# Performance work log

Hardware: AMD Instinct MI355X
Metric: run time of the kernel (lower is better)

## Reference

```python
import jax, jax.numpy as jnp
import numpy as np

D_MODEL = 1024
N_HEADS = 16
D_HEAD = D_MODEL // N_HEADS


def setup_inputs() -> dict:
    key = jax.random.key(0)
    ks = jax.random.split(key, 9)
    B, S = 2, 2048
    s = 0.02
    return {
        "x": jax.random.normal(ks[0], (B, S, D_MODEL), dtype=jnp.float32),
        "Wq": jax.random.normal(ks[1], (D_MODEL, D_MODEL), dtype=jnp.float32) * s,
        "bq": jnp.zeros((D_MODEL,), dtype=jnp.float32),
        "Wk": jax.random.normal(ks[2], (D_MODEL, D_MODEL), dtype=jnp.float32) * s,
        "bk": jnp.zeros((D_MODEL,), dtype=jnp.float32),
        "Wv": jax.random.normal(ks[3], (D_MODEL, D_MODEL), dtype=jnp.float32) * s,
        "bv": jnp.zeros((D_MODEL,), dtype=jnp.float32),
        "Wo": jax.random.normal(ks[4], (D_MODEL, D_MODEL), dtype=jnp.float32) * s,
        "bo": jnp.zeros((D_MODEL,), dtype=jnp.float32),
    }


def reference(x, Wq, bq, Wk, bk, Wv, bv, Wo, bo):
    B, S, _ = x.shape
    # projections -> [B, H, S, Dh]
    def split_heads(t):
        return t.reshape(B, S, N_HEADS, D_HEAD).transpose(0, 2, 1, 3)
    Q = split_heads(x @ Wq + bq)
    K = split_heads(x @ Wk + bk)
    V = split_heads(x @ Wv + bv)
    scores = jnp.einsum('bhqd,bhkd->bhqk', Q, K)  # [B,H,S,S]
    mask = jnp.tril(jnp.ones((S, S), dtype=bool))
    # NB: original masks BEFORE scaling (mask fill -1e9 then /sqrt(d_head))
    scores = jnp.where(mask[None, None], scores, jnp.float32(-1e9))
    scores = scores / jnp.sqrt(jnp.float32(D_HEAD))
    attn = jax.nn.softmax(scores, axis=-1)
    ctx = jnp.einsum('bhqk,bhkd->bhqd', attn, V)
    ctx = ctx.transpose(0, 2, 1, 3).reshape(B, S, D_MODEL)
    return ctx @ Wo + bo
```

## Files before the change

kernel.cpp:

```cpp
#include <hip/hip_runtime.h>

typedef __bf16 bf16;
typedef __bf16 bf16x8 __attribute__((ext_vector_type(8)));
typedef __bf16 bf16x4 __attribute__((ext_vector_type(4)));
typedef float  f32x4  __attribute__((ext_vector_type(4)));

#define D_MODEL 1024
#define S_LEN   2048
#define NHEAD   16
#define DHEAD   64
#define BATCH   2
#define MROWS   (BATCH * S_LEN)

#define QSCALE 0.18033688011112042f

__device__ __forceinline__ void gld_lds16(const void* g, void* lds_base) {
    __builtin_amdgcn_global_load_lds(
        (const __attribute__((address_space(1))) void*)g,
        (__attribute__((address_space(3))) void*)lds_base, 16, 0, 0);
}

__global__ void prep_kernel(const float* __restrict__ x,
                            const float* __restrict__ W0, const float* __restrict__ W1,
                            const float* __restrict__ W2, const float* __restrict__ W3,
                            bf16* __restrict__ xb, bf16* __restrict__ Wt) {
    int tx = threadIdx.x, ty = threadIdx.y;
    if (blockIdx.z == 4) {
        int tid = ty * 32 + tx;
        size_t base = ((size_t)blockIdx.y * 32 + blockIdx.x) * 4096;
#pragma unroll
        for (int j = 0; j < 4; j++) {
            size_t i = base + (size_t)(j * 256 + tid) * 4;
            f32x4 v = *(const f32x4*)(x + i);
            bf16x4 o;
            o[0] = (bf16)v[0]; o[1] = (bf16)v[1]; o[2] = (bf16)v[2]; o[3] = (bf16)v[3];
            *(bf16x4*)(xb + i) = o;
        }
        return;
    }
    __shared__ float tile[32][33];
    const float* W = (blockIdx.z == 0) ? W0 : (blockIdx.z == 1) ? W1
                   : (blockIdx.z == 2) ? W2 : W3;
    int n0 = blockIdx.x * 32, k0 = blockIdx.y * 32;
#pragma unroll
    for (int j = 0; j < 4; j++)
        tile[ty + 8 * j][tx] = W[(size_t)(k0 + ty + 8 * j) * D_MODEL + n0 + tx];
    __syncthreads();
    bf16* out = Wt + (size_t)blockIdx.z * D_MODEL * D_MODEL;
#pragma unroll
    for (int j = 0; j < 4; j++)
        out[(size_t)(n0 + ty + 8 * j) * D_MODEL + k0 + tx] = (bf16)tile[tx][ty + 8 * j];
}

template <int MODE>
__global__ __launch_bounds__(256, 3) void gemm_kernel(
    const bf16* __restrict__ A, const bf16* __restrict__ Bt,
    const float* __restrict__ b0, const float* __restrict__ b1, const float* __restrict__ b2,
    bf16* __restrict__ Qo, bf16* __restrict__ Ko, bf16* __restrict__ Vto,
    float* __restrict__ Co) {
    constexpr int BN = (MODE == 0) ? 128 : 64;
    constexpr int MI = (MODE == 0) ? 4 : 2;
    __shared__ bf16 sA[3][128 * 32];
    __shared__ bf16 sB[3][BN * 32];
    const int t = threadIdx.x;
    const int wave = t >> 6, lane = t & 63;
    const int quad = lane >> 4, m16 = lane & 15;
    const int wrow = (MODE == 0) ? (wave >> 1) * 64 : wave * 32;
    const int wcol = (MODE == 0) ? (wave & 1) * 64 : 0;
    const int row0 = blockIdx.y * 128, col0 = blockIdx.x * BN;
    const int K = D_MODEL;
    constexpr int NK = D_MODEL / 32;

    f32x4 acc[MI][4];
#pragma unroll
    for (int i = 0; i < MI; i++)
#pragma unroll
        for (int j = 0; j < 4; j++) acc[i][j] = (f32x4){0.f, 0.f, 0.f, 0.f};

    auto stage = [&](int kk, int buf) {
#pragma unroll
        for (int i = 0; i < 2; i++) {
            int cb = i * 256 + wave * 64;
            int c  = cb + lane;
            int r  = c >> 2, kg = c & 3;
            int gk = kg ^ ((r >> 1) & 3);
            gld_lds16(A + (size_t)(row0 + r) * K + kk * 32 + gk * 8,
                      (char*)&sA[buf][0] + cb * 16);
        }
#pragma unroll
        for (int i = 0; i < BN / 64; i++) {
            int cb = i * 256 + wave * 64;
            int c  = cb + lane;
            int r  = c >> 2, kg = c & 3;
            int gk = kg ^ ((r >> 1) & 3);
            gld_lds16(Bt + (size_t)(col0 + r) * K + kk * 32 + gk * 8,
                      (char*)&sB[buf][0] + cb * 16);
        }
    };

    stage(0, 0);
    stage(1, 1);

    const int sx = (m16 >> 1) & 3;
    for (int ks = 0; ks < NK; ++ks) {
        if (ks + 1 < NK) {
            if constexpr (MODE == 0)
                asm volatile("s_waitcnt vmcnt(4)\n\ts_barrier" ::: "memory");
            else
                asm volatile("s_waitcnt vmcnt(3)\n\ts_barrier" ::: "memory");
        } else {
            asm volatile("s_waitcnt vmcnt(0)\n\ts_barrier" ::: "memory");
        }
        if (ks + 2 < NK) stage(ks + 2, (ks + 2) % 3);

        const int cur = ks % 3;
        const int gg = (quad ^ sx) * 8;
        bf16x8 af[MI], bfr[4];
#pragma unroll
        for (int mi = 0; mi < MI; mi++)
            af[mi] = *(const bf16x8*)&sA[cur][(wrow + mi * 16 + m16) * 32 + gg];
#pragma unroll
        for (int ni = 0; ni < 4; ni++)
            bfr[ni] = *(const bf16x8*)&sB[cur][(wcol + ni * 16 + m16) * 32 + gg];
#pragma unroll
        for (int mi = 0; mi < MI; mi++)
#pragma unroll
            for (int ni = 0; ni < 4; ni++)
                acc[mi][ni] = __builtin_amdgcn_mfma_f32_16x16x32_bf16(
                    af[mi], bfr[ni], acc[mi][ni], 0, 0, 0);
    }

    if (MODE == 1) {
#pragma unroll
        for (int mi = 0; mi < MI; mi++) {
            int r0 = row0 + wrow + mi * 16 + quad * 4;
#pragma unroll
            for (int ni = 0; ni < 4; ni++) {
                int col = col0 + wcol + ni * 16 + m16;
                float bias = b0[col];
#pragma unroll
                for (int r = 0; r < 4; r++)
                    Co[(size_t)(r0 + r) * D_MODEL + col] = acc[mi][ni][r] + bias;
            }
        }
    } else {
        int sel = col0 >> 10;
        const float* bias_arr = (sel == 0) ? b0 : (sel == 1) ? b1 : b2;
#pragma unroll
        for (int mi = 0; mi < MI; mi++) {
            int s0g = row0 + wrow + mi * 16 + quad * 4;
            int b = s0g >> 11, ss0 = s0g & 2047;
#pragma unroll
            for (int ni = 0; ni < 4; ni++) {
                int col = col0 + wcol + ni * 16 + m16;
                int cn = col & 1023;
                int h = cn >> 6, d = cn & 63;
                float bias = bias_arr[cn];
                if (sel < 2) {
                    bf16* dst = (sel == 0) ? Qo : Ko;
                    float scl = (sel == 0) ? QSCALE : 1.0f;
                    size_t base = (((size_t)b * NHEAD + h) * S_LEN);
#pragma unroll
                    for (int r = 0; r < 4; r++)
                        dst[(base + ss0 + r) * DHEAD + d] = (bf16)((acc[mi][ni][r] + bias) * scl);
                } else {
                    bf16x4 pk;
#pragma unroll
                    for (int r = 0; r < 4; r++) pk[r] = (bf16)(acc[mi][ni][r] + bias);
                    *(bf16x4*)(Vto + (((size_t)b * NHEAD + h) * DHEAD + d) * S_LEN + ss0) = pk;
                }
            }
        }
    }
}

__global__ __launch_bounds__(256, 4) void attn_kernel(
    const bf16* __restrict__ Q, const bf16* __restrict__ K,
    const bf16* __restrict__ Vt, bf16* __restrict__ ctx) {
    __shared__ bf16 Kt_s[2][64 * 64];
    __shared__ bf16 Vt_s[2][64 * 64];

    const int t = threadIdx.x, wave = t >> 6, lane = t & 63;
    const int quad = lane >> 4, m16 = lane & 15;
    const int bh = blockIdx.x;
    const int qt = 31 - blockIdx.y;
    const int nt = qt + 1;
    const size_t base = (size_t)bh * S_LEN * DHEAD;

    bf16x8 aq[2];
#pragma unroll
    for (int kst = 0; kst < 2; kst++)
        aq[kst] = *(const bf16x8*)(Q + base
            + (size_t)(qt * 64 + wave * 16 + m16) * DHEAD + kst * 32 + quad * 8);

    f32x4 o[4];
#pragma unroll
    for (int di = 0; di < 4; di++) o[di] = (f32x4){0.f, 0.f, 0.f, 0.f};
    float l_acc = 0.f;

    auto stage = [&](int j, int buf) {
#pragma unroll
        for (int i = 0; i < 2; i++) {
            int cb = i * 256 + wave * 64;
            int c  = cb + lane;
            int pos = c >> 3, g = c & 7;
            int gk = g ^ (pos & 7);
            gld_lds16(K  + base + (size_t)(j * 64 + pos) * DHEAD + gk * 8,
                      (char*)&Kt_s[buf][0] + cb * 16);
            gld_lds16(Vt + base + (size_t)pos * S_LEN + j * 64 + gk * 8,
                      (char*)&Vt_s[buf][0] + cb * 16);
        }
    };

    stage(0, 0);

    for (int j = 0; j < nt; ++j) {
        asm volatile("s_waitcnt vmcnt(0)\n\ts_barrier" ::: "memory");
        if (j + 1 < nt) stage(j + 1, (j + 1) & 1);

        const int cur = j & 1;
        const int kt0 = j * 64;

        f32x4 sc[4];
#pragma unroll
        for (int ni = 0; ni < 4; ni++) sc[ni] = (f32x4){0.f, 0.f, 0.f, 0.f};
        __builtin_amdgcn_s_setprio(1);
#pragma unroll
        for (int ni = 0; ni < 4; ni++) {
            int pos = ni * 16 + m16;
#pragma unroll
            for (int kst = 0; kst < 2; kst++) {
                int gg = (kst * 4 + quad) ^ (pos & 7);
                bf16x8 kf = *(const bf16x8*)&Kt_s[cur][pos * 64 + gg * 8];
                sc[ni] = __builtin_amdgcn_mfma_f32_16x16x32_bf16(
                    kf, aq[kst], sc[ni], 0, 0, 0);
            }
        }
        __builtin_amdgcn_s_setprio(0);

        if (j == qt) {
            int qg = qt * 64 + wave * 16 + m16;
#pragma unroll
            for (int ni = 0; ni < 4; ni++)
#pragma unroll
                for (int r = 0; r < 4; r++) {
                    int kp = kt0 + ni * 16 + quad * 4 + r;
                    if (kp > qg) sc[ni][r] = -1e9f;
                }
        }

        unsigned int pd[4][2];
        {
            float ls0 = 0.f, ls1 = 0.f;
#pragma unroll
            for (int ni = 0; ni < 4; ni++) {
                float p0 = __builtin_amdgcn_exp2f(sc[ni][0]);
                float p1 = __builtin_amdgcn_exp2f(sc[ni][1]);
                float p2 = __builtin_amdgcn_exp2f(sc[ni][2]);
                float p3 = __builtin_amdgcn_exp2f(sc[ni][3]);
                union { bf16x4 h; unsigned int u[2]; } cv;
                cv.h[0] = (bf16)p0; cv.h[1] = (bf16)p1;
                cv.h[2] = (bf16)p2; cv.h[3] = (bf16)p3;
                pd[ni][0] = cv.u[0];
                pd[ni][1] = cv.u[1];
                ls0 += p0 + p1;
                ls1 += p2 + p3;
            }
            l_acc += ls0 + ls1;
        }

#pragma unroll
        for (int kst = 0; kst < 2; kst++) {
            unsigned int x0 = pd[2 * kst][0],     y0 = pd[2 * kst][1];
            unsigned int x1 = pd[2 * kst + 1][0], y1 = pd[2 * kst + 1][1];
            asm("v_permlane32_swap_b32 %0, %1" : "+v"(x0), "+v"(x1));
            asm("v_permlane32_swap_b32 %0, %1" : "+v"(y0), "+v"(y1));
            asm("v_permlane16_swap_b32 %0, %1" : "+v"(x0), "+v"(x1));
            asm("v_permlane16_swap_b32 %0, %1" : "+v"(y0), "+v"(y1));
            union { unsigned int u[4]; bf16x8 v; } pk;
            pk.u[0] = x0; pk.u[1] = y0; pk.u[2] = x1; pk.u[3] = y1;
            bf16x8 ap = pk.v;
            __builtin_amdgcn_s_setprio(1);
#pragma unroll
            for (int di = 0; di < 4; di++) {
                int d = di * 16 + m16;
                int gg = (kst * 4 + quad) ^ (d & 7);
                bf16x8 vf = *(const bf16x8*)&Vt_s[cur][d * 64 + gg * 8];
                o[di] = __builtin_amdgcn_mfma_f32_16x16x32_bf16(
                    vf, ap, o[di], 0, 0, 0);
            }
            __builtin_amdgcn_s_setprio(0);
        }
    }

    int b = bh >> 4, h = bh & 15;
    float l = l_acc;
    l += __shfl_xor(l, 16);
    l += __shfl_xor(l, 32);
    float rl = 1.0f / l;
    int s = qt * 64 + wave * 16 + m16;
#pragma unroll
    for (int di = 0; di < 4; di++) {
        bf16x4 pk;
#pragma unroll
        for (int r = 0; r < 4; r++) pk[r] = (bf16)(o[di][r] * rl);
        *(bf16x4*)(ctx + ((size_t)b * S_LEN + s) * D_MODEL
                   + h * DHEAD + di * 16 + quad * 4) = pk;
    }
}

extern "C" void kernel_launch(void* const* d_in, const int* in_sizes, int n_in,
                              void* d_out, int out_size, void* d_ws, size_t ws_size,
                              hipStream_t stream) {
    const float* x  = (const float*)d_in[0];
    const float* Wq = (const float*)d_in[1];
    const float* bq = (const float*)d_in[2];
    const float* Wk = (const float*)d_in[3];
    const float* bk = (const float*)d_in[4];
    const float* Wv = (const float*)d_in[5];
    const float* bv = (const float*)d_in[6];
    const float* Wo = (const float*)d_in[7];
    const float* bo = (const float*)d_in[8];
    float* out = (float*)d_out;

    char* ws = (char*)d_ws;
    const size_t MB = 1u << 20;
    bf16* xb  = (bf16*)(ws + 0);
    bf16* Wt  = (bf16*)(ws + 8  * MB);
    bf16* Qb  = (bf16*)(ws + 16 * MB);
    bf16* Kb  = (bf16*)(ws + 24 * MB);
    bf16* Vtb = (bf16*)(ws + 32 * MB);
    bf16* ctx = (bf16*)(ws + 0);

    prep_kernel<<<dim3(32, 32, 5), dim3(32, 8), 0, stream>>>(x, Wq, Wk, Wv, Wo, xb, Wt);
    gemm_kernel<0><<<dim3(24, 32), 256, 0, stream>>>(xb, Wt, bq, bk, bv,
                                                     Qb, Kb, Vtb, nullptr);
    attn_kernel<<<dim3(32, 32), 256, 0, stream>>>(Qb, Kb, Vtb, ctx);
    gemm_kernel<1><<<dim3(16, 32), 256, 0, stream>>>(ctx, Wt + 3 * 1024 * 1024,
                                                     bo, nullptr, nullptr,
                                                     nullptr, nullptr, nullptr, out);
}
```

Before: 178.8 us.

## Retile QKV GEMM to 128x64 BK64 and split-K output projection in-block

```diff
diff --git a/kernel.cpp b/kernel.cpp
--- a/kernel.cpp
+++ b/kernel.cpp
@@ -52,49 +52,147 @@
         out[(size_t)(n0 + ty + 8 * j) * D_MODEL + k0 + tx] = (bf16)tile[tx][ty + 8 * j];
 }
 
-template <int MODE>
-__global__ __launch_bounds__(256, 3) void gemm_kernel(
+__global__ __launch_bounds__(256, 3) void gemm0_kernel(
     const bf16* __restrict__ A, const bf16* __restrict__ Bt,
     const float* __restrict__ b0, const float* __restrict__ b1, const float* __restrict__ b2,
-    bf16* __restrict__ Qo, bf16* __restrict__ Ko, bf16* __restrict__ Vto,
-    float* __restrict__ Co) {
-    constexpr int BN = (MODE == 0) ? 128 : 64;
-    constexpr int MI = (MODE == 0) ? 4 : 2;
-    __shared__ bf16 sA[3][128 * 32];
-    __shared__ bf16 sB[3][BN * 32];
+    bf16* __restrict__ Qo, bf16* __restrict__ Ko, bf16* __restrict__ Vto) {
+    __shared__ bf16 sA[2][128 * 64];
+    __shared__ bf16 sB[2][64 * 64];
     const int t = threadIdx.x;
     const int wave = t >> 6, lane = t & 63;
     const int quad = lane >> 4, m16 = lane & 15;
-    const int wrow = (MODE == 0) ? (wave >> 1) * 64 : wave * 32;
-    const int wcol = (MODE == 0) ? (wave & 1) * 64 : 0;
-    const int row0 = blockIdx.y * 128, col0 = blockIdx.x * BN;
-    const int K = D_MODEL;
-    constexpr int NK = D_MODEL / 32;
-
-    f32x4 acc[MI][4];
-#pragma unroll
-    for (int i = 0; i < MI; i++)
+    const int wrow = wave * 32;
+    const int row0 = blockIdx.y * 128, col0 = blockIdx.x * 64;
+    constexpr int NK = D_MODEL / 64;
+
+    f32x4 acc[2][4];
+#pragma unroll
+    for (int i = 0; i < 2; i++)
 #pragma unroll
         for (int j = 0; j < 4; j++) acc[i][j] = (f32x4){0.f, 0.f, 0.f, 0.f};
 
     auto stage = [&](int kk, int buf) {
+#pragma unroll
+        for (int i = 0; i < 4; i++) {
+            int cb = i * 256 + wave * 64;
+            int c  = cb + lane;
+            int r  = c >> 3, sl = c & 7;
+            int gk = sl ^ (r & 7);
+            gld_lds16(A + (size_t)(row0 + r) * D_MODEL + kk * 64 + gk * 8,
+                      (char*)&sA[buf][0] + cb * 16);
+        }
 #pragma unroll
         for (int i = 0; i < 2; i++) {
             int cb = i * 256 + wave * 64;
             int c  = cb + lane;
-            int r  = c >> 2, kg = c & 3;
-            int gk = kg ^ ((r >> 1) & 3);
-            gld_lds16(A + (size_t)(row0 + r) * K + kk * 32 + gk * 8,
-                      (char*)&sA[buf][0] + cb * 16);
-        }
-#pragma unroll
-        for (int i = 0; i < BN / 64; i++) {
-            int cb = i * 256 + wave * 64;
+            int r  = c >> 3, sl = c & 7;
+            int gk = sl ^ (r & 7);
+            gld_lds16(Bt + (size_t)(col0 + r) * D_MODEL + kk * 64 + gk * 8,
+                      (char*)&sB[buf][0] + cb * 16);
+        }
+    };
+
+    stage(0, 0);
+
+    const int s7 = m16 & 7;
+    for (int ks = 0; ks < NK; ++ks) {
+        asm volatile("s_waitcnt vmcnt(0)\n\ts_barrier" ::: "memory");
+        if (ks + 1 < NK) stage(ks + 1, (ks + 1) & 1);
+
+        const int cur = ks & 1;
+        bf16x8 af[2][2], bfr[4][2];
+#pragma unroll
+        for (int mi = 0; mi < 2; mi++)
+#pragma unroll
+            for (int kst = 0; kst < 2; kst++) {
+                int g = kst * 4 + quad;
+                af[mi][kst] = *(const bf16x8*)
+                    &sA[cur][(wrow + mi * 16 + m16) * 64 + (g ^ s7) * 8];
+            }
+#pragma unroll
+        for (int ni = 0; ni < 4; ni++)
+#pragma unroll
+            for (int kst = 0; kst < 2; kst++) {
+                int g = kst * 4 + quad;
+                bfr[ni][kst] = *(const bf16x8*)
+                    &sB[cur][(ni * 16 + m16) * 64 + (g ^ s7) * 8];
+            }
+#pragma unroll
+        for (int kst = 0; kst < 2; kst++)
+#pragma unroll
+            for (int mi = 0; mi < 2; mi++)
+#pragma unroll
+                for (int ni = 0; ni < 4; ni++)
+                    acc[mi][ni] = __builtin_amdgcn_mfma_f32_16x16x32_bf16(
+                        af[mi][kst], bfr[ni][kst], acc[mi][ni], 0, 0, 0);
+    }
+
+    int sel = col0 >> 10;
+    const float* bias_arr = (sel == 0) ? b0 : (sel == 1) ? b1 : b2;
+#pragma unroll
+    for (int mi = 0; mi < 2; mi++) {
+        int s0g = row0 + wrow + mi * 16 + quad * 4;
+        int b = s0g >> 11, ss0 = s0g & 2047;
+#pragma unroll
+        for (int ni = 0; ni < 4; ni++) {
+            int col = col0 + ni * 16 + m16;
+            int cn = col & 1023;
+            int h = cn >> 6, d = cn & 63;
+            float bias = bias_arr[cn];
+            if (sel < 2) {
+                bf16* dst = (sel == 0) ? Qo : Ko;
+                float scl = (sel == 0) ? QSCALE : 1.0f;
+                size_t base = (((size_t)b * NHEAD + h) * S_LEN);
+#pragma unroll
+                for (int r = 0; r < 4; r++)
+                    dst[(base + ss0 + r) * DHEAD + d] = (bf16)((acc[mi][ni][r] + bias) * scl);
+            } else {
+                bf16x4 pk;
+#pragma unroll
+                for (int r = 0; r < 4; r++) pk[r] = (bf16)(acc[mi][ni][r] + bias);
+                *(bf16x4*)(Vto + (((size_t)b * NHEAD + h) * DHEAD + d) * S_LEN + ss0) = pk;
+            }
+        }
+    }
+}
+
+__global__ __launch_bounds__(512, 4) void gemm1_kernel(
+    const bf16* __restrict__ A, const bf16* __restrict__ Bt,
+    const float* __restrict__ bias, float* __restrict__ Co) {
+    __shared__ bf16 sA[3][2][128 * 32];
+    __shared__ bf16 sB[3][2][64 * 32];
+    const int t = threadIdx.x;
+    const int wave = t >> 6, lane = t & 63;
+    const int quad = lane >> 4, m16 = lane & 15;
+    const int grp = wave >> 2, w4 = wave & 3;
+    const int wrow = w4 * 32;
+    const int row0 = blockIdx.y * 128, col0 = blockIdx.x * 64;
+    const int kbase = grp * 512;
+    constexpr int NK = 16;
+
+    f32x4 acc[2][4];
+#pragma unroll
+    for (int i = 0; i < 2; i++)
+#pragma unroll
+        for (int j = 0; j < 4; j++) acc[i][j] = (f32x4){0.f, 0.f, 0.f, 0.f};
+
+    auto stage = [&](int kk, int buf) {
+#pragma unroll
+        for (int i = 0; i < 2; i++) {
+            int cb = i * 256 + w4 * 64;
             int c  = cb + lane;
             int r  = c >> 2, kg = c & 3;
             int gk = kg ^ ((r >> 1) & 3);
-            gld_lds16(Bt + (size_t)(col0 + r) * K + kk * 32 + gk * 8,
-                      (char*)&sB[buf][0] + cb * 16);
+            gld_lds16(A + (size_t)(row0 + r) * D_MODEL + kbase + kk * 32 + gk * 8,
+                      (char*)&sA[buf][grp][0] + cb * 16);
+        }
+        {
+            int cb = w4 * 64;
+            int c  = cb + lane;
+            int r  = c >> 2, kg = c & 3;
+            int gk = kg ^ ((r >> 1) & 3);
+            gld_lds16(Bt + (size_t)(col0 + r) * D_MODEL + kbase + kk * 32 + gk * 8,
+                      (char*)&sB[buf][grp][0] + cb * 16);
         }
     };
 
@@ -103,74 +201,56 @@
 
     const int sx = (m16 >> 1) & 3;
     for (int ks = 0; ks < NK; ++ks) {
-        if (ks + 1 < NK) {
-            if constexpr (MODE == 0)
-                asm volatile("s_waitcnt vmcnt(4)\n\ts_barrier" ::: "memory");
-            else
-                asm volatile("s_waitcnt vmcnt(3)\n\ts_barrier" ::: "memory");
-        } else {
+        if (ks + 1 < NK)
+            asm volatile("s_waitcnt vmcnt(3)\n\ts_barrier" ::: "memory");
+        else
             asm volatile("s_waitcnt vmcnt(0)\n\ts_barrier" ::: "memory");
-        }
         if (ks + 2 < NK) stage(ks + 2, (ks + 2) % 3);
 
         const int cur = ks % 3;
         const int gg = (quad ^ sx) * 8;
-        bf16x8 af[MI], bfr[4];
-#pragma unroll
-        for (int mi = 0; mi < MI; mi++)
-            af[mi] = *(const bf16x8*)&sA[cur][(wrow + mi * 16 + m16) * 32 + gg];
+        bf16x8 af[2], bfr[4];
+#pragma unroll
+        for (int mi = 0; mi < 2; mi++)
+            af[mi] = *(const bf16x8*)&sA[cur][grp][(wrow + mi * 16 + m16) * 32 + gg];
 #pragma unroll
         for (int ni = 0; ni < 4; ni++)
-            bfr[ni] = *(const bf16x8*)&sB[cur][(wcol + ni * 16 + m16) * 32 + gg];
-#pragma unroll
-        for (int mi = 0; mi < MI; mi++)
+            bfr[ni] = *(const bf16x8*)&sB[cur][grp][(ni * 16 + m16) * 32 + gg];
+#pragma unroll
+        for (int mi = 0; mi < 2; mi++)
 #pragma unroll
             for (int ni = 0; ni < 4; ni++)
                 acc[mi][ni] = __builtin_amdgcn_mfma_f32_16x16x32_bf16(
                     af[mi], bfr[ni], acc[mi][ni], 0, 0, 0);
     }
 
-    if (MODE == 1) {
-#pragma unroll
-        for (int mi = 0; mi < MI; mi++) {
-            int r0 = row0 + wrow + mi * 16 + quad * 4;
+    __syncthreads();
+    float* scr = (float*)&sA[0][0][0];
+    if (grp == 1) {
+#pragma unroll
+        for (int mi = 0; mi < 2; mi++)
+#pragma unroll
+            for (int ni = 0; ni < 4; ni++)
+#pragma unroll
+                for (int r = 0; r < 4; r++)
+                    scr[(wrow + mi * 16 + quad * 4 + r) * 66 + ni * 16 + m16] =
+                        acc[mi][ni][r];
+    }
+    __syncthreads();
+    if (grp == 0) {
+#pragma unroll
+        for (int mi = 0; mi < 2; mi++)
 #pragma unroll
             for (int ni = 0; ni < 4; ni++) {
-                int col = col0 + wcol + ni * 16 + m16;
-                float bias = b0[col];
-#pragma unroll
-                for (int r = 0; r < 4; r++)
-                    Co[(size_t)(r0 + r) * D_MODEL + col] = acc[mi][ni][r] + bias;
-            }
-        }
-    } else {
-        int sel = col0 >> 10;
-        const float* bias_arr = (sel == 0) ? b0 : (sel == 1) ? b1 : b2;
-#pragma unroll
-        for (int mi = 0; mi < MI; mi++) {
-            int s0g = row0 + wrow + mi * 16 + quad * 4;
-            int b = s0g >> 11, ss0 = s0g & 2047;
-#pragma unroll
-            for (int ni = 0; ni < 4; ni++) {
-                int col = col0 + wcol + ni * 16 + m16;
-                int cn = col & 1023;
-                int h = cn >> 6, d = cn & 63;
-                float bias = bias_arr[cn];
-                if (sel < 2) {
-                    bf16* dst = (sel == 0) ? Qo : Ko;
-                    float scl = (sel == 0) ? QSCALE : 1.0f;
-                    size_t base = (((size_t)b * NHEAD + h) * S_LEN);
-#pragma unroll
-                    for (int r = 0; r < 4; r++)
-                        dst[(base + ss0 + r) * DHEAD + d] = (bf16)((acc[mi][ni][r] + bias) * scl);
-                } else {
-                    bf16x4 pk;
-#pragma unroll
-                    for (int r = 0; r < 4; r++) pk[r] = (bf16)(acc[mi][ni][r] + bias);
-                    *(bf16x4*)(Vto + (((size_t)b * NHEAD + h) * DHEAD + d) * S_LEN + ss0) = pk;
+                int col = col0 + ni * 16 + m16;
+                float bb = bias[col];
+#pragma unroll
+                for (int r = 0; r < 4; r++) {
+                    int row = wrow + mi * 16 + quad * 4 + r;
+                    Co[(size_t)(row0 + row) * D_MODEL + col] =
+                        acc[mi][ni][r] + scr[row * 66 + ni * 16 + m16] + bb;
                 }
             }
-        }
     }
 }
 
@@ -333,10 +413,9 @@
     bf16* ctx = (bf16*)(ws + 0);
 
     prep_kernel<<<dim3(32, 32, 5), dim3(32, 8), 0, stream>>>(x, Wq, Wk, Wv, Wo, xb, Wt);
-    gemm_kernel<0><<<dim3(24, 32), 256, 0, stream>>>(xb, Wt, bq, bk, bv,
-                                                     Qb, Kb, Vtb, nullptr);
+    gemm0_kernel<<<dim3(48, 32), 256, 0, stream>>>(xb, Wt, bq, bk, bv,
+                                                   Qb, Kb, Vtb);
     attn_kernel<<<dim3(32, 32), 256, 0, stream>>>(Qb, Kb, Vtb, ctx);
-    gemm_kernel<1><<<dim3(16, 32), 256, 0, stream>>>(ctx, Wt + 3 * 1024 * 1024,
-                                                     bo, nullptr, nullptr,
-                                                     nullptr, nullptr, nullptr, out);
-}
+    gemm1_kernel<<<dim3(16, 32), 512, 0, stream>>>(ctx, Wt + 3 * 1024 * 1024,
+                                                   bo, out);
+}
```

Result: no change. 177.4 us (-0.8%).

## Split-K output projection with atomic accumulation and 128x128 tiles

Applied to the files above, without the earlier changes.

```diff
diff --git a/kernel.cpp b/kernel.cpp
--- a/kernel.cpp
+++ b/kernel.cpp
@@ -23,8 +23,18 @@
 __global__ void prep_kernel(const float* __restrict__ x,
                             const float* __restrict__ W0, const float* __restrict__ W1,
                             const float* __restrict__ W2, const float* __restrict__ W3,
-                            bf16* __restrict__ xb, bf16* __restrict__ Wt) {
+                            bf16* __restrict__ xb, bf16* __restrict__ Wt,
+                            float* __restrict__ outz) {
     int tx = threadIdx.x, ty = threadIdx.y;
+    if (blockIdx.z == 5) {
+        int tid = ty * 32 + tx;
+        size_t base = ((size_t)blockIdx.y * 32 + blockIdx.x) * 4096;
+#pragma unroll
+        for (int j = 0; j < 4; j++)
+            *(f32x4*)(outz + base + (size_t)(j * 256 + tid) * 4) =
+                (f32x4){0.f, 0.f, 0.f, 0.f};
+        return;
+    }
     if (blockIdx.z == 4) {
         int tid = ty * 32 + tx;
         size_t base = ((size_t)blockIdx.y * 32 + blockIdx.x) * 4096;
@@ -52,28 +62,22 @@
         out[(size_t)(n0 + ty + 8 * j) * D_MODEL + k0 + tx] = (bf16)tile[tx][ty + 8 * j];
 }
 
-template <int MODE>
-__global__ __launch_bounds__(256, 3) void gemm_kernel(
+__global__ __launch_bounds__(256, 3) void gemm0_kernel(
     const bf16* __restrict__ A, const bf16* __restrict__ Bt,
     const float* __restrict__ b0, const float* __restrict__ b1, const float* __restrict__ b2,
-    bf16* __restrict__ Qo, bf16* __restrict__ Ko, bf16* __restrict__ Vto,
-    float* __restrict__ Co) {
-    constexpr int BN = (MODE == 0) ? 128 : 64;
-    constexpr int MI = (MODE == 0) ? 4 : 2;
+    bf16* __restrict__ Qo, bf16* __restrict__ Ko, bf16* __restrict__ Vto) {
     __shared__ bf16 sA[3][128 * 32];
-    __shared__ bf16 sB[3][BN * 32];
+    __shared__ bf16 sB[3][128 * 32];
     const int t = threadIdx.x;
     const int wave = t >> 6, lane = t & 63;
     const int quad = lane >> 4, m16 = lane & 15;
-    const int wrow = (MODE == 0) ? (wave >> 1) * 64 : wave * 32;
-    const int wcol = (MODE == 0) ? (wave & 1) * 64 : 0;
-    const int row0 = blockIdx.y * 128, col0 = blockIdx.x * BN;
-    const int K = D_MODEL;
+    const int wrow = (wave >> 1) * 64, wcol = (wave & 1) * 64;
+    const int row0 = blockIdx.y * 128, col0 = blockIdx.x * 128;
     constexpr int NK = D_MODEL / 32;
 
-    f32x4 acc[MI][4];
-#pragma unroll
-    for (int i = 0; i < MI; i++)
+    f32x4 acc[4][4];
+#pragma unroll
+    for (int i = 0; i < 4; i++)
 #pragma unroll
         for (int j = 0; j < 4; j++) acc[i][j] = (f32x4){0.f, 0.f, 0.f, 0.f};
 
@@ -84,16 +88,16 @@
             int c  = cb + lane;
             int r  = c >> 2, kg = c & 3;
             int gk = kg ^ ((r >> 1) & 3);
-            gld_lds16(A + (size_t)(row0 + r) * K + kk * 32 + gk * 8,
+            gld_lds16(A + (size_t)(row0 + r) * D_MODEL + kk * 32 + gk * 8,
                       (char*)&sA[buf][0] + cb * 16);
         }
 #pragma unroll
-        for (int i = 0; i < BN / 64; i++) {
+        for (int i = 0; i < 2; i++) {
             int cb = i * 256 + wave * 64;
             int c  = cb + lane;
             int r  = c >> 2, kg = c & 3;
             int gk = kg ^ ((r >> 1) & 3);
-            gld_lds16(Bt + (size_t)(col0 + r) * K + kk * 32 + gk * 8,
+            gld_lds16(Bt + (size_t)(col0 + r) * D_MODEL + kk * 32 + gk * 8,
                       (char*)&sB[buf][0] + cb * 16);
         }
     };
@@ -103,73 +107,134 @@
 
     const int sx = (m16 >> 1) & 3;
     for (int ks = 0; ks < NK; ++ks) {
-        if (ks + 1 < NK) {
-            if constexpr (MODE == 0)
-                asm volatile("s_waitcnt vmcnt(4)\n\ts_barrier" ::: "memory");
-            else
-                asm volatile("s_waitcnt vmcnt(3)\n\ts_barrier" ::: "memory");
-        } else {
+        if (ks + 1 < NK)
+            asm volatile("s_waitcnt vmcnt(4)\n\ts_barrier" ::: "memory");
+        else
             asm volatile("s_waitcnt vmcnt(0)\n\ts_barrier" ::: "memory");
-        }
         if (ks + 2 < NK) stage(ks + 2, (ks + 2) % 3);
 
         const int cur = ks % 3;
         const int gg = (quad ^ sx) * 8;
-        bf16x8 af[MI], bfr[4];
-#pragma unroll
-        for (int mi = 0; mi < MI; mi++)
+        bf16x8 af[4], bfr[4];
+#pragma unroll
+        for (int mi = 0; mi < 4; mi++)
             af[mi] = *(const bf16x8*)&sA[cur][(wrow + mi * 16 + m16) * 32 + gg];
 #pragma unroll
         for (int ni = 0; ni < 4; ni++)
             bfr[ni] = *(const bf16x8*)&sB[cur][(wcol + ni * 16 + m16) * 32 + gg];
 #pragma unroll
-        for (int mi = 0; mi < MI; mi++)
+        for (int mi = 0; mi < 4; mi++)
 #pragma unroll
             for (int ni = 0; ni < 4; ni++)
                 acc[mi][ni] = __builtin_amdgcn_mfma_f32_16x16x32_bf16(
                     af[mi], bfr[ni], acc[mi][ni], 0, 0, 0);
     }
 
-    if (MODE == 1) {
-#pragma unroll
-        for (int mi = 0; mi < MI; mi++) {
-            int r0 = row0 + wrow + mi * 16 + quad * 4;
-#pragma unroll
-            for (int ni = 0; ni < 4; ni++) {
-                int col = col0 + wcol + ni * 16 + m16;
-                float bias = b0[col];
+    int sel = col0 >> 10;
+    const float* bias_arr = (sel == 0) ? b0 : (sel == 1) ? b1 : b2;
+#pragma unroll
+    for (int mi = 0; mi < 4; mi++) {
+        int s0g = row0 + wrow + mi * 16 + quad * 4;
+        int b = s0g >> 11, ss0 = s0g & 2047;
+#pragma unroll
+        for (int ni = 0; ni < 4; ni++) {
+            int col = col0 + wcol + ni * 16 + m16;
+            int cn = col & 1023;
+            int h = cn >> 6, d = cn & 63;
+            float bias = bias_arr[cn];
+            if (sel < 2) {
+                bf16* dst = (sel == 0) ? Qo : Ko;
+                float scl = (sel == 0) ? QSCALE : 1.0f;
+                size_t base = (((size_t)b * NHEAD + h) * S_LEN);
 #pragma unroll
                 for (int r = 0; r < 4; r++)
-                    Co[(size_t)(r0 + r) * D_MODEL + col] = acc[mi][ni][r] + bias;
+                    dst[(base + ss0 + r) * DHEAD + d] = (bf16)((acc[mi][ni][r] + bias) * scl);
+            } else {
+                bf16x4 pk;
+#pragma unroll
+                for (int r = 0; r < 4; r++) pk[r] = (bf16)(acc[mi][ni][r] + bias);
+                *(bf16x4*)(Vto + (((size_t)b * NHEAD + h) * DHEAD + d) * S_LEN + ss0) = pk;
             }
         }
-    } else {
-        int sel = col0 >> 10;
-        const float* bias_arr = (sel == 0) ? b0 : (sel == 1) ? b1 : b2;
-#pragma unroll
-        for (int mi = 0; mi < MI; mi++) {
-            int s0g = row0 + wrow + mi * 16 + quad * 4;
-            int b = s0g >> 11, ss0 = s0g & 2047;
-#pragma unroll
-            for (int ni = 0; ni < 4; ni++) {
-                int col = col0 + wcol + ni * 16 + m16;
-                int cn = col & 1023;
-                int h = cn >> 6, d = cn & 63;
-                float bias = bias_arr[cn];
-                if (sel < 2) {
-                    bf16* dst = (sel == 0) ? Qo : Ko;
-                    float scl = (sel == 0) ? QSCALE : 1.0f;
-                    size_t base = (((size_t)b * NHEAD + h) * S_LEN);
-#pragma unroll
-                    for (int r = 0; r < 4; r++)
-                        dst[(base + ss0 + r) * DHEAD + d] = (bf16)((acc[mi][ni][r] + bias) * scl);
-                } else {
-                    bf16x4 pk;
-#pragma unroll
-                    for (int r = 0; r < 4; r++) pk[r] = (bf16)(acc[mi][ni][r] + bias);
-                    *(bf16x4*)(Vto + (((size_t)b * NHEAD + h) * DHEAD + d) * S_LEN + ss0) = pk;
-                }
-            }
+    }
+}
+
+__global__ __launch_bounds__(256, 4) void gemm1_kernel(
+    const bf16* __restrict__ A, const bf16* __restrict__ Bt,
+    const float* __restrict__ bias, float* __restrict__ Co) {
+    __shared__ bf16 sA[2][128 * 32];
+    __shared__ bf16 sB[2][128 * 32];
+    const int t = threadIdx.x;
+    const int wave = t >> 6, lane = t & 63;
+    const int quad = lane >> 4, m16 = lane & 15;
+    const int wrow = (wave >> 1) * 64, wcol = (wave & 1) * 64;
+    const int row0 = blockIdx.y * 128, col0 = blockIdx.x * 128;
+    const int kbase = blockIdx.z * 256;
+    constexpr int NK = 8;
+
+    f32x4 acc[4][4];
+#pragma unroll
+    for (int i = 0; i < 4; i++)
+#pragma unroll
+        for (int j = 0; j < 4; j++) acc[i][j] = (f32x4){0.f, 0.f, 0.f, 0.f};
+
+    auto stage = [&](int kk, int buf) {
+#pragma unroll
+        for (int i = 0; i < 2; i++) {
+            int cb = i * 256 + wave * 64;
+            int c  = cb + lane;
+            int r  = c >> 2, kg = c & 3;
+            int gk = kg ^ ((r >> 1) & 3);
+            gld_lds16(A + (size_t)(row0 + r) * D_MODEL + kbase + kk * 32 + gk * 8,
+                      (char*)&sA[buf][0] + cb * 16);
+        }
+#pragma unroll
+        for (int i = 0; i < 2; i++) {
+            int cb = i * 256 + wave * 64;
+            int c  = cb + lane;
+            int r  = c >> 2, kg = c & 3;
+            int gk = kg ^ ((r >> 1) & 3);
+            gld_lds16(Bt + (size_t)(col0 + r) * D_MODEL + kbase + kk * 32 + gk * 8,
+                      (char*)&sB[buf][0] + cb * 16);
+        }
+    };
+
+    stage(0, 0);
+
+    const int sx = (m16 >> 1) & 3;
+    for (int ks = 0; ks < NK; ++ks) {
+        asm volatile("s_waitcnt vmcnt(0)\n\ts_barrier" ::: "memory");
+        if (ks + 1 < NK) stage(ks + 1, (ks + 1) & 1);
+
+        const int cur = ks & 1;
+        const int gg = (quad ^ sx) * 8;
+        bf16x8 af[4], bfr[4];
+#pragma unroll
+        for (int mi = 0; mi < 4; mi++)
+            af[mi] = *(const bf16x8*)&sA[cur][(wrow + mi * 16 + m16) * 32 + gg];
+#pragma unroll
+        for (int ni = 0; ni < 4; ni++)
+            bfr[ni] = *(const bf16x8*)&sB[cur][(wcol + ni * 16 + m16) * 32 + gg];
+#pragma unroll
+        for (int mi = 0; mi < 4; mi++)
+#pragma unroll
+            for (int ni = 0; ni < 4; ni++)
+                acc[mi][ni] = __builtin_amdgcn_mfma_f32_16x16x32_bf16(
+                    af[mi], bfr[ni], acc[mi][ni], 0, 0, 0);
+    }
+
+    const bool g0 = (blockIdx.z == 0);
+#pragma unroll
+    for (int mi = 0; mi < 4; mi++) {
+        int r0 = row0 + wrow + mi * 16 + quad * 4;
+#pragma unroll
+        for (int ni = 0; ni < 4; ni++) {
+            int col = col0 + wcol + ni * 16 + m16;
+            float bb = g0 ? bias[col] : 0.f;
+#pragma unroll
+            for (int r = 0; r < 4; r++)
+                atomicAdd(&Co[(size_t)(r0 + r) * D_MODEL + col],
+                          acc[mi][ni][r] + bb);
         }
     }
 }
@@ -332,11 +397,11 @@
     bf16* Vtb = (bf16*)(ws + 32 * MB);
     bf16* ctx = (bf16*)(ws + 0);
 
-    prep_kernel<<<dim3(32, 32, 5), dim3(32, 8), 0, stream>>>(x, Wq, Wk, Wv, Wo, xb, Wt);
-    gemm_kernel<0><<<dim3(24, 32), 256, 0, stream>>>(xb, Wt, bq, bk, bv,
-                                                     Qb, Kb, Vtb, nullptr);
+    prep_kernel<<<dim3(32, 32, 6), dim3(32, 8), 0, stream>>>(x, Wq, Wk, Wv, Wo,
+                                                             xb, Wt, out);
+    gemm0_kernel<<<dim3(24, 32), 256, 0, stream>>>(xb, Wt, bq, bk, bv,
+                                                   Qb, Kb, Vtb);
     attn_kernel<<<dim3(32, 32), 256, 0, stream>>>(Qb, Kb, Vtb, ctx);
-    gemm_kernel<1><<<dim3(16, 32), 256, 0, stream>>>(ctx, Wt + 3 * 1024 * 1024,
-                                                     bo, nullptr, nullptr,
-                                                     nullptr, nullptr, nullptr, out);
-}
+    gemm1_kernel<<<dim3(8, 32, 4), 256, 0, stream>>>(ctx, Wt + 3 * 1024 * 1024,
+                                                     bo, out);
+}
```

New measurement: 225.0 us. +25.8%, slower.
